# Optimization experiments

Measured on AMD Instinct MI355X. Metric: run time of the kernel, lower is better.

## Reference

```python
import jax, jax.numpy as jnp
import numpy as np

B, T, TA = 16, 512, 1024
D_REG, D_AUD, HID, HEADS = 512, 512, 256, 4
NREG = 4  # mouth, left_eye, right_eye, nose (dict order)
N = NREG * B * T + B * TA  # total graph nodes


def _build_edges():
    # Faithful, vectorized version of build_graph's edge construction (phoneme_times=None).
    bs = np.arange(B)[:, None]
    ts = np.arange(T)[None, :]
    src, dst = [], []
    # cross-region same-timestep edges, all ordered pairs i != j (edge_attr 0)
    for i in range(NREG):
        for j in range(NREG):
            if i != j:
                n1 = i * B * T + bs * T + ts
                n2 = j * B * T + bs * T + ts
                src.append(n1.ravel()); dst.append(n2.ravel())
    # temporal edges within each region (edge_attr 1)
    tt = np.arange(T - 1)[None, :]
    for i in range(NREG):
        n1 = i * B * T + bs * T + tt
        src.append(n1.ravel()); dst.append((n1 + 1).ravel())
    # eye (region idx 1,2) -> audio alignment edges (edge_attr 3)
    t_aud = (np.arange(T)[None, :] * TA) // T
    audio_start = NREG * B * T
    for i in (1, 2):
        n_eye = i * B * T + bs * T + ts
        n_aud = audio_start + bs * TA + t_aud
        src.append(n_eye.ravel()); dst.append(np.broadcast_to(n_aud, (B, T)).ravel())
    # self loops (PyG GATConv default add_self_loops=True)
    loops = np.arange(N)
    src.append(loops); dst.append(loops)
    return np.concatenate(src).astype(np.int32), np.concatenate(dst).astype(np.int32)


def setup_inputs() -> dict:
    key = jax.random.key(0)
    ks = iter(jax.random.split(key, 48))
    def rn(shape, scale=1.0):
        return jax.random.normal(next(ks), shape, dtype=jnp.float32) * jnp.float32(scale)
    src_np, dst_np = _build_edges()
    inp = {
        'mouth': rn((B, T, D_REG)), 'left_eye': rn((B, T, D_REG)),
        'right_eye': rn((B, T, D_REG)), 'nose': rn((B, T, D_REG)),
        'audio_embeddings': rn((B, TA, D_AUD)),
    }
    s = 1.0 / np.sqrt(D_REG)
    for name in ['mouth', 'left_eye', 'right_eye', 'nose']:
        inp['w_' + name] = rn((D_REG, HID), s)
        inp['b_' + name] = jnp.zeros((HID,), jnp.float32)
    inp['w_audio'] = rn((D_AUD, HID), 1.0 / np.sqrt(D_AUD))
    inp['b_audio'] = jnp.zeros((HID,), jnp.float32)
    # GAT layers: layer 0 in=HID, layers 1,2 in=HID*HEADS; layers 0,1 concat, layer 2 averages heads
    dims_in = [HID, HID * HEADS, HID * HEADS]
    for l, din in enumerate(dims_in):
        concat = l < 2
        inp[f'W{l}'] = rn((din, HEADS * HID), 1.0 / np.sqrt(din))
        inp[f'as{l}'] = rn((HEADS, HID), 0.1)
        inp[f'ad{l}'] = rn((HEADS, HID), 0.1)
        inp[f'bias{l}'] = jnp.zeros((HEADS * HID,) if concat else (HID,), jnp.float32)
    inp['ln_g'] = jnp.ones((HID,), jnp.float32)
    inp['ln_b'] = jnp.zeros((HID,), jnp.float32)
    inp['src'] = jnp.asarray(src_np)
    inp['dst'] = jnp.asarray(dst_np)
    return inp


def _gat(x, W, a_s, a_d, bias, src, dst, concat):
    # PyG GATConv (eval mode): gather -> per-head attention softmax over dst -> scatter-add
    H, C = a_s.shape
    h = (x @ W).reshape(-1, H, C)                      # [N,H,C]
    alpha_s = jnp.sum(h * a_s, -1)                     # [N,H]
    alpha_d = jnp.sum(h * a_d, -1)                     # [N,H]
    e = jax.nn.leaky_relu(alpha_s[src] + alpha_d[dst], 0.2)  # [E,H]
    m = jax.ops.segment_max(e, dst, num_segments=N)
    ex = jnp.exp(e - m[dst])
    denom = jax.ops.segment_sum(ex, dst, num_segments=N)
    alpha = ex / (denom[dst] + jnp.float32(1e-16))
    out = jax.ops.segment_sum(h[src] * alpha[:, :, None], dst, num_segments=N)  # [N,H,C]
    out = out.reshape(-1, H * C) if concat else out.mean(1)
    return out + bias


def _forward(mouth, left_eye, right_eye, nose, audio_embeddings,
             w_mouth, b_mouth, w_left_eye, b_left_eye, w_right_eye, b_right_eye,
             w_nose, b_nose, w_audio, b_audio,
             W0, as0, ad0, bias0, W1, as1, ad1, bias1, W2, as2, ad2, bias2,
             ln_g, ln_b, src, dst):
    x = jnp.concatenate([
        (mouth @ w_mouth + b_mouth).reshape(B * T, HID),
        (left_eye @ w_left_eye + b_left_eye).reshape(B * T, HID),
        (right_eye @ w_right_eye + b_right_eye).reshape(B * T, HID),
        (nose @ w_nose + b_nose).reshape(B * T, HID),
        (audio_embeddings @ w_audio + b_audio).reshape(B * TA, HID),
    ], axis=0)                                          # [N,HID]
    x = _gat(x, W0, as0, ad0, bias0, src, dst, True)    # [N,HID*HEADS]
    x = _gat(x, W1, as1, ad1, bias1, src, dst, True)    # [N,HID*HEADS]
    x = _gat(x, W2, as2, ad2, bias2, src, dst, False)   # [N,HID]
    mu = x.mean(-1, keepdims=True)
    var = jnp.mean(jnp.square(x - mu), -1, keepdims=True)
    x = (x - mu) / jnp.sqrt(var + jnp.float32(1e-5)) * ln_g + ln_b
    nodes_pb = NREG * T + TA
    return x.reshape(B, nodes_pb, HID).mean(1)          # [B,HID]


def reference(mouth, left_eye, right_eye, nose, audio_embeddings,
              w_mouth, b_mouth, w_left_eye, b_left_eye, w_right_eye, b_right_eye,
              w_nose, b_nose, w_audio, b_audio,
              W0, as0, ad0, bias0, W1, as1, ad1, bias1, W2, as2, ad2, bias2,
              ln_g, ln_b, src, dst):
    return _forward(mouth, left_eye, right_eye, nose, audio_embeddings,
                    w_mouth, b_mouth, w_left_eye, b_left_eye, w_right_eye, b_right_eye,
                    w_nose, b_nose, w_audio, b_audio,
                    W0, as0, ad0, bias0, W1, as1, ad1, bias1, W2, as2, ad2, bias2,
                    ln_g, ln_b, src, dst)
```

## Files before the change

kernel.cpp:

```cpp
#include <hip/hip_runtime.h>


typedef unsigned short u16;
typedef unsigned int u32;
typedef __bf16 bf16x8 __attribute__((ext_vector_type(8)));
typedef float f32x4 __attribute__((ext_vector_type(4)));

#define ASYNC16(gp, lp)                                                        \
  __builtin_amdgcn_global_load_lds(                                            \
      (const __attribute__((address_space(1))) void*)(gp),                     \
      (__attribute__((address_space(3))) void*)(lp), 16, 0, 0)

__device__ __forceinline__ u16 f2bf(float f) {
  union { float f; u32 u; } v; v.f = f;
  u32 u = v.u + 0x7FFFu + ((v.u >> 16) & 1u);
  return (u16)(u >> 16);
}
__device__ __forceinline__ float bf2f(u16 x) {
  union { u32 u; float f; } v; v.u = ((u32)x) << 16;
  return v.f;
}
__device__ __forceinline__ float4 load_bf4(const u16* p) {
  ushort4 s = *(const ushort4*)p;
  float4 r; r.x = bf2f(s.x); r.y = bf2f(s.y); r.z = bf2f(s.z); r.w = bf2f(s.w);
  return r;
}
__device__ __forceinline__ float lrelu(float v) { return v > 0.f ? v : 0.2f * v; }
__device__ __forceinline__ float dot4(float4 a, float4 b) {
  return a.x * b.x + a.y * b.y + a.z * b.z + a.w * b.w;
}
__device__ __forceinline__ float wred(float v) {
#pragma unroll
  for (int off = 32; off; off >>= 1) v += __shfl_down(v, off);
  return v;
}
__device__ __forceinline__ float wredx(float v) {
#pragma unroll
  for (int off = 32; off; off >>= 1) v += __shfl_xor(v, off);
  return v;
}

struct PK { const float* W[8]; u16* P[8]; int KB[8]; int NN[8]; int st[9]; };
__global__ __launch_bounds__(256) void pack_kernel(PK p) {
  const int f = blockIdx.x * 4 + (threadIdx.x >> 6);
  const int lane = threadIdx.x & 63;
  int e = 0;
  while (f >= p.st[e + 1]) ++e;
  const int local = f - p.st[e];
  const int KB = p.KB[e], N = p.NN[e];
  const int nt = local / KB, kb = local % KB;
  const float* W = p.W[e] + (size_t)(kb * 32 + (lane >> 4) * 8) * N + nt * 16 + (lane & 15);
  u16* dst = p.P[e] + ((size_t)local * 64 + lane) * 8;
  u16 o[8];
#pragma unroll
  for (int j = 0; j < 8; ++j) o[j] = f2bf(W[(size_t)j * N]);
  *(uint4*)dst = *(uint4*)o;
}

__global__ __launch_bounds__(256) void gemm_kernel(
    const u16* __restrict__ A, const u16* __restrict__ Bp, u16* __restrict__ C,
    int K, int ldc) {
  __shared__ __align__(16) u16 As[2][2][128 * 32];
  const int KB = K >> 5;
  const int KB2 = K >> 6;
  const int w = blockIdx.y * 8 + blockIdx.x;
  const int xcd = w & 7, m = w >> 3;
  const int blockCol = (m & 7) * 128;
  const int blockRow = ((m >> 3) * 8 + xcd) * 128;
  const int tid = threadIdx.x;
  const int wave = tid >> 6, lane = tid & 63;
  const int wr = (wave >> 1) * 64, wc = (wave & 1) * 64;
  const int lr = lane & 15, lq = lane >> 4;
  const int sRow = wave * 16 + (lane >> 2);
  const int sGc = (lane & 3) ^ ((sRow >> 1) & 3);
  const size_t aOff0 = (size_t)(blockRow + sRow) * K + sGc * 8;
  const size_t aOff1 = aOff0 + (size_t)64 * K;
  const int ldsOff0 = wave * 512;
  const int ldsOff1 = 2048 + wave * 512;

  const u16* Bn[4];
#pragma unroll
  for (int ni = 0; ni < 4; ++ni)
    Bn[ni] = Bp + ((size_t)(((blockCol + wc) >> 4) + ni) * KB) * 512 + lane * 8;

  f32x4 acc[4][4] = {};

#pragma unroll
  for (int h = 0; h < 2; ++h) {
    ASYNC16(A + aOff0 + h * 32, As[0][h] + ldsOff0);
    ASYNC16(A + aOff1 + h * 32, As[0][h] + ldsOff1);
  }
  __syncthreads();

  for (int kb2 = 0; kb2 < KB2; ++kb2) {
    const int cb = kb2 & 1;
    if (kb2 + 1 < KB2) {
      const size_t k1 = (size_t)(kb2 + 1) * 64;
#pragma unroll
      for (int h = 0; h < 2; ++h) {
        ASYNC16(A + aOff0 + k1 + h * 32, As[cb ^ 1][h] + ldsOff0);
        ASYNC16(A + aOff1 + k1 + h * 32, As[cb ^ 1][h] + ldsOff1);
      }
    }
#pragma unroll
    for (int h = 0; h < 2; ++h) {
      const int kb = kb2 * 2 + h;
      const u16* cur = As[cb][h];
      bf16x8 bfr[4];
#pragma unroll
      for (int ni = 0; ni < 4; ++ni)
        bfr[ni] = *(const bf16x8*)(Bn[ni] + (size_t)kb * 512);
      bf16x8 af[4];
#pragma unroll
      for (int mi = 0; mi < 4; ++mi) {
        const int R = wr + mi * 16 + lr;
        const int cp = lq ^ ((R >> 1) & 3);
        af[mi] = *(const bf16x8*)(cur + R * 32 + cp * 8);
      }
#pragma unroll
      for (int mi = 0; mi < 4; ++mi)
#pragma unroll
        for (int ni = 0; ni < 4; ++ni)
          acc[mi][ni] = __builtin_amdgcn_mfma_f32_16x16x32_bf16(af[mi], bfr[ni],
                                                                acc[mi][ni], 0, 0, 0);
    }
    __syncthreads();
  }
#pragma unroll
  for (int mi = 0; mi < 4; ++mi)
#pragma unroll
    for (int ni = 0; ni < 4; ++ni) {
      const int col = blockCol + wc + ni * 16 + lr;
#pragma unroll
      for (int r = 0; r < 4; ++r) {
        const int row = blockRow + wr + mi * 16 + lq * 4 + r;
        C[(size_t)row * ldc + col] = f2bf(acc[mi][ni][r]);
      }
    }
}

struct ProjArgs { const float* x[5]; const u16* w[5]; const float* b[5]; };
__global__ __launch_bounds__(256) void proj_kernel(ProjArgs pa,
                                                   u16* __restrict__ C) {
  __shared__ __align__(16) u16 As[128 * 32];
  const int blockRow = blockIdx.y * 128, blockCol = blockIdx.x * 128;
  const int reg = blockRow >= 32768 ? 4 : (blockRow >> 13);
  const int regBase = reg == 4 ? 32768 : reg * 8192;
  const float* Af = pa.x[reg] + (size_t)(blockRow - regBase) * 512;
  const u16* Bp = pa.w[reg];
  const int tid = threadIdx.x;
  const int wave = tid >> 6, lane = tid & 63;
  const int wr = (wave >> 1) * 64, wc = (wave & 1) * 64;
  const int lr = lane & 15, lq = lane >> 4;
  const int rr = tid >> 2;
  const int cphys = tid & 3;
  const int sGc = cphys ^ ((tid >> 3) & 3);

  const u16* Bn[4];
#pragma unroll
  for (int ni = 0; ni < 4; ++ni)
    Bn[ni] = Bp + ((size_t)(((blockCol + wc) >> 4) + ni) * 16) * 512 + lane * 8;

  f32x4 acc[4][4] = {};

  for (int k0 = 0; k0 < 512; k0 += 32) {
    __syncthreads();
    bf16x8 bfr[4];
#pragma unroll
    for (int ni = 0; ni < 4; ++ni)
      bfr[ni] = *(const bf16x8*)(Bn[ni] + (size_t)k0 * 16);
#pragma unroll
    for (int i = 0; i < 2; ++i) {
      const int row = i * 64 + rr;
      const float* ap = Af + (size_t)row * 512 + k0 + sGc * 8;
      float4 f0 = *(const float4*)(ap);
      float4 f1 = *(const float4*)(ap + 4);
      uint4 pk;
      pk.x = (u32)f2bf(f0.x) | ((u32)f2bf(f0.y) << 16);
      pk.y = (u32)f2bf(f0.z) | ((u32)f2bf(f0.w) << 16);
      pk.z = (u32)f2bf(f1.x) | ((u32)f2bf(f1.y) << 16);
      pk.w = (u32)f2bf(f1.z) | ((u32)f2bf(f1.w) << 16);
      *(uint4*)(&As[row * 32 + cphys * 8]) = pk;
    }
    __syncthreads();
    bf16x8 af[4];
#pragma unroll
    for (int mi = 0; mi < 4; ++mi) {
      const int R = wr + mi * 16 + lr;
      const int cp = lq ^ ((R >> 1) & 3);
      af[mi] = *(const bf16x8*)(&As[R * 32 + cp * 8]);
    }
#pragma unroll
    for (int mi = 0; mi < 4; ++mi)
#pragma unroll
      for (int ni = 0; ni < 4; ++ni)
        acc[mi][ni] = __builtin_amdgcn_mfma_f32_16x16x32_bf16(af[mi], bfr[ni],
                                                              acc[mi][ni], 0, 0, 0);
  }
  const float* bias = pa.b[reg];
#pragma unroll
  for (int mi = 0; mi < 4; ++mi)
#pragma unroll
    for (int ni = 0; ni < 4; ++ni) {
      const int col = blockCol + wc + ni * 16 + lr;
      const float bv = bias[col];
#pragma unroll
      for (int r = 0; r < 4; ++r) {
        const int row = blockRow + wr + mi * 16 + lq * 4 + r;
        C[(size_t)row * 256 + col] = f2bf(acc[mi][ni][r] + bv);
      }
    }
}

template <bool MEAN>
__global__ __launch_bounds__(256) void agg_kernel(
    const u16* __restrict__ h, const float* __restrict__ a_s,
    const float* __restrict__ a_d, const float* __restrict__ bias,
    const float* __restrict__ lng, const float* __restrict__ lnb,
    void* __restrict__ out) {
  const int tid = threadIdx.x;
  const int head = tid >> 6, lane = tid & 63;
  const int c4 = tid * 4;
  const float4 sa = *(const float4*)(a_s + c4);
  const float4 da = *(const float4*)(a_d + c4);
  __shared__ float asB[2][4][4], adL[4][4], alpha[4][4][5];
  __shared__ float red[MEAN ? 4096 : 1];
  __shared__ float ls[MEAN ? 32 : 1];

  if (blockIdx.x < 1024) {
    const int b = blockIdx.x >> 6;
    const int t0 = (blockIdx.x & 63) * 8;
    float4 hprev[4] = {};
    if (t0 > 0) {
      const int btp = b * 512 + t0 - 1;
#pragma unroll
      for (int r = 0; r < 4; ++r) {
        hprev[r] = load_bf4(h + (size_t)(r * 8192 + btp) * 1024 + c4);
        float sp = wred(dot4(hprev[r], sa));
        if (lane == 0) asB[1][r][head] = sp;
      }
    }
    __syncthreads();
    float pacc[4] = {};
    int pch[4] = {-1, -1, -1, -1};
    for (int tt = 0; tt < 8; ++tt) {
      const int t = t0 + tt, bt = b * 512 + t;
      const bool hasPrev = (t > 0);
      float4 hv[4];
#pragma unroll
      for (int r = 0; r < 4; ++r) {
        hv[r] = load_bf4(h + (size_t)(r * 8192 + bt) * 1024 + c4);
        float ss = wred(dot4(hv[r], sa));
        float dd = wred(dot4(hv[r], da));
        if (lane == 0) { asB[tt & 1][r][head] = ss; adL[r][head] = dd; }
      }
      __syncthreads();
      if (tid < 16) {
        const int j = tid >> 2, hh = tid & 3;
        const float ad = adL[j][hh];
        float e[5];
#pragma unroll
        for (int r = 0; r < 4; ++r) e[r] = lrelu(asB[tt & 1][r][hh] + ad);
        int cnt = 4;
        if (hasPrev) { e[4] = lrelu(asB[(tt & 1) ^ 1][j][hh] + ad); cnt = 5; }
        float mx = e[0];
        for (int k = 1; k < cnt; ++k) mx = fmaxf(mx, e[k]);
        float s = 0.f, ex[5];
        for (int k = 0; k < cnt; ++k) { ex[k] = __expf(e[k] - mx); s += ex[k]; }
        const float inv = 1.f / (s + 1e-16f);
#pragma unroll
        for (int k = 0; k < 5; ++k) alpha[j][hh][k] = (k < cnt) ? ex[k] * inv : 0.f;
      }
      __syncthreads();
#pragma unroll
      for (int j = 0; j < 4; ++j) {
        const float* al = &alpha[j][head][0];
        float4 acc;
        acc.x = al[0] * hv[0].x + al[1] * hv[1].x + al[2] * hv[2].x + al[3] * hv[3].x;
        acc.y = al[0] * hv[0].y + al[1] * hv[1].y + al[2] * hv[2].y + al[3] * hv[3].y;
        acc.z = al[0] * hv[0].z + al[1] * hv[1].z + al[2] * hv[2].z + al[3] * hv[3].z;
        acc.w = al[0] * hv[0].w + al[1] * hv[1].w + al[2] * hv[2].w + al[3] * hv[3].w;
        if (hasPrev) {
          const float a4 = al[4];
          acc.x += a4 * hprev[j].x; acc.y += a4 * hprev[j].y;
          acc.z += a4 * hprev[j].z; acc.w += a4 * hprev[j].w;
        }
        if constexpr (!MEAN) {
          const float4 bv = *(const float4*)(bias + c4);
          ushort4 o;
          o.x = f2bf(acc.x + bv.x); o.y = f2bf(acc.y + bv.y);
          o.z = f2bf(acc.z + bv.z); o.w = f2bf(acc.w + bv.w);
          *(ushort4*)((u16*)out + (size_t)(j * 8192 + bt) * 1024 + c4) = o;
        } else {
          *(float4*)(&red[j * 1024 + c4]) = acc;
        }
      }
      if constexpr (MEAN) {
        __syncthreads();
        const float bb = bias[tid];
        float v[4];
#pragma unroll
        for (int j = 0; j < 4; ++j) {
          v[j] = 0.25f * (red[j * 1024 + tid] + red[j * 1024 + tid + 256] +
                          red[j * 1024 + tid + 512] + red[j * 1024 + tid + 768]) + bb;
          const float sj = wredx(v[j]);
          const float qj = wredx(v[j] * v[j]);
          if (lane == 0) { ls[head * 8 + j * 2] = sj; ls[head * 8 + j * 2 + 1] = qj; }
        }
        __syncthreads();
#pragma unroll
        for (int j = 0; j < 4; ++j) {
          const float S = ls[j * 2] + ls[8 + j * 2] + ls[16 + j * 2] + ls[24 + j * 2];
          const float Q = ls[j * 2 + 1] + ls[8 + j * 2 + 1] + ls[16 + j * 2 + 1] +
                          ls[24 + j * 2 + 1];
          const float mean = S * (1.f / 256.f);
          const float var = Q * (1.f / 256.f) - mean * mean;
          const float n = (v[j] - mean) * rsqrtf(var + 1e-5f) * lng[tid] + lnb[tid];
          const int ch = (j * 8192 + bt) / 3072;
          if (ch != pch[j]) {
            if (pch[j] >= 0) atomicAdd((float*)out + pch[j] * 256 + tid, pacc[j]);
            pacc[j] = 0.f; pch[j] = ch;
          }
          pacc[j] += n;
        }
      }
#pragma unroll
      for (int r = 0; r < 4; ++r) hprev[r] = hv[r];
    }
    if constexpr (MEAN) {
#pragma unroll
      for (int j = 0; j < 4; ++j)
        if (pch[j] >= 0) atomicAdd((float*)out + pch[j] * 256 + tid, pacc[j]);
    }
  } else {
    const int aid = blockIdx.x - 1024;
    const int idx0 = aid * 2;
    const int b = idx0 >> 10;
    const int ta0 = idx0 & 1023;
    const int n0 = 32768 + idx0, n1 = n0 + 1;
    const int tt2 = ta0 >> 1;
    const int le = 8192 + b * 512 + tt2;
    const int re = 16384 + b * 512 + tt2;
    float4 v0 = load_bf4(h + (size_t)n0 * 1024 + c4);
    float4 vo = load_bf4(h + (size_t)n1 * 1024 + c4);
    float4 v1 = load_bf4(h + (size_t)le * 1024 + c4);
    float4 v2 = load_bf4(h + (size_t)re * 1024 + c4);
    {
      float s0 = wred(dot4(v0, sa));
      float s1 = wred(dot4(v1, sa));
      float s2 = wred(dot4(v2, sa));
      float d0 = wred(dot4(v0, da));
      if (lane == 0) {
        asB[0][0][head] = s0; asB[0][1][head] = s1; asB[0][2][head] = s2;
        adL[0][head] = d0;
      }
    }
    __syncthreads();
    if (tid < 4) {
      const float ad = adL[0][tid];
      float e0 = lrelu(asB[0][0][tid] + ad);
      float e1 = lrelu(asB[0][1][tid] + ad);
      float e2 = lrelu(asB[0][2][tid] + ad);
      float mx = fmaxf(e0, fmaxf(e1, e2));
      float x0 = __expf(e0 - mx), x1 = __expf(e1 - mx), x2 = __expf(e2 - mx);
      float inv = 1.f / (x0 + x1 + x2 + 1e-16f);
      alpha[0][tid][0] = x0 * inv; alpha[0][tid][1] = x1 * inv;
      alpha[0][tid][2] = x2 * inv;
    }
    __syncthreads();
    const float a0 = alpha[0][head][0], a1 = alpha[0][head][1], a2 = alpha[0][head][2];
    v0.x = a0 * v0.x + a1 * v1.x + a2 * v2.x;
    v0.y = a0 * v0.y + a1 * v1.y + a2 * v2.y;
    v0.z = a0 * v0.z + a1 * v1.z + a2 * v2.z;
    v0.w = a0 * v0.w + a1 * v1.w + a2 * v2.w;
    if constexpr (!MEAN) {
      const float4 bv = *(const float4*)(bias + c4);
      ushort4 oe, oo;
      oe.x = f2bf(v0.x + bv.x); oe.y = f2bf(v0.y + bv.y);
      oe.z = f2bf(v0.z + bv.z); oe.w = f2bf(v0.w + bv.w);
      oo.x = f2bf(vo.x + bv.x); oo.y = f2bf(vo.y + bv.y);
      oo.z = f2bf(vo.z + bv.z); oo.w = f2bf(vo.w + bv.w);
      *(ushort4*)((u16*)out + (size_t)n0 * 1024 + c4) = oe;
      *(ushort4*)((u16*)out + (size_t)n1 * 1024 + c4) = oo;
    } else {
      *(float4*)(&red[c4]) = v0;
      *(float4*)(&red[1024 + c4]) = vo;
      __syncthreads();
      const float bb = bias[tid];
      float vA = 0.25f * (red[tid] + red[tid + 256] + red[tid + 512] + red[tid + 768]) + bb;
      float vB = 0.25f * (red[1024 + tid] + red[1024 + tid + 256] +
                          red[1024 + tid + 512] + red[1024 + tid + 768]) + bb;
      const float sA = wredx(vA), qA = wredx(vA * vA);
      const float sB = wredx(vB), qB = wredx(vB * vB);
      if (lane == 0) {
        ls[head * 8] = sA; ls[head * 8 + 1] = qA;
        ls[head * 8 + 2] = sB; ls[head * 8 + 3] = qB;
      }
      __syncthreads();
      const float SA = ls[0] + ls[8] + ls[16] + ls[24];
      const float QA = ls[1] + ls[9] + ls[17] + ls[25];
      const float SB = ls[2] + ls[10] + ls[18] + ls[26];
      const float QB = ls[3] + ls[11] + ls[19] + ls[27];
      const float mA = SA * (1.f / 256.f), vrA = QA * (1.f / 256.f) - mA * mA;
      const float mB = SB * (1.f / 256.f), vrB = QB * (1.f / 256.f) - mB * mB;
      const float g = lng[tid], be = lnb[tid];
      const float nA = (vA - mA) * rsqrtf(vrA + 1e-5f) * g + be;
      const float nB = (vB - mB) * rsqrtf(vrB + 1e-5f) * g + be;
      const int ch0 = n0 / 3072, ch1 = n1 / 3072;
      if (ch0 == ch1) {
        atomicAdd((float*)out + ch0 * 256 + tid, nA + nB);
      } else {
        atomicAdd((float*)out + ch0 * 256 + tid, nA);
        atomicAdd((float*)out + ch1 * 256 + tid, nB);
      }
    }
  }
}

__global__ __launch_bounds__(256) void zero_kernel(float* __restrict__ p) {
  p[blockIdx.x * 256 + threadIdx.x] = 0.f;
}
__global__ __launch_bounds__(256) void scale_kernel(float* __restrict__ p) {
  const int i = blockIdx.x * 256 + threadIdx.x;
  p[i] *= (1.f / 3072.f);
}

extern "C" void kernel_launch(void* const* d_in, const int* in_sizes, int n_in,
                              void* d_out, int out_size, void* d_ws, size_t ws_size,
                              hipStream_t stream) {
  const float* x_reg[4] = {(const float*)d_in[0], (const float*)d_in[1],
                           (const float*)d_in[2], (const float*)d_in[3]};
  const float* audio = (const float*)d_in[4];
  const float* w_reg[4] = {(const float*)d_in[5], (const float*)d_in[7],
                           (const float*)d_in[9], (const float*)d_in[11]};
  const float* b_reg[4] = {(const float*)d_in[6], (const float*)d_in[8],
                           (const float*)d_in[10], (const float*)d_in[12]};
  const float* w_aud = (const float*)d_in[13];
  const float* b_aud = (const float*)d_in[14];
  const float* Wl[3] = {(const float*)d_in[15], (const float*)d_in[19],
                        (const float*)d_in[23]};
  const float* as_in[3] = {(const float*)d_in[16], (const float*)d_in[20],
                           (const float*)d_in[24]};
  const float* ad_in[3] = {(const float*)d_in[17], (const float*)d_in[21],
                           (const float*)d_in[25]};
  const float* bias_l[3] = {(const float*)d_in[18], (const float*)d_in[22],
                            (const float*)d_in[26]};
  const float* ln_g = (const float*)d_in[27];
  const float* ln_b = (const float*)d_in[28];

  char* ws = (char*)d_ws;
  u16* h_bf = (u16*)ws;
  u16* xb = (u16*)(ws + 100663296);
  u16* wt = (u16*)(ws + 201326592);

  u16* wtp[5];
  for (int r = 0; r < 5; ++r) wtp[r] = wt + (size_t)r * 131072;
  u16* wt0 = wt + 655360;
  u16* wt1 = wt + 917504;
  u16* wt2 = wt + 1966080;

  PK pk;
  for (int r = 0; r < 4; ++r) { pk.W[r] = w_reg[r]; pk.P[r] = wtp[r]; pk.KB[r] = 16; pk.NN[r] = 256; }
  pk.W[4] = w_aud; pk.P[4] = wtp[4]; pk.KB[4] = 16; pk.NN[4] = 256;
  pk.W[5] = Wl[0]; pk.P[5] = wt0; pk.KB[5] = 8;  pk.NN[5] = 1024;
  pk.W[6] = Wl[1]; pk.P[6] = wt1; pk.KB[6] = 32; pk.NN[6] = 1024;
  pk.W[7] = Wl[2]; pk.P[7] = wt2; pk.KB[7] = 32; pk.NN[7] = 1024;
  pk.st[0] = 0;
  {
    const int nfr[8] = {256, 256, 256, 256, 256, 512, 2048, 2048};
    int acc = 0;
    for (int e = 0; e < 8; ++e) { acc += nfr[e]; pk.st[e + 1] = acc; }
  }
  pack_kernel<<<pk.st[8] / 4, 256, 0, stream>>>(pk);
  zero_kernel<<<16, 256, 0, stream>>>((float*)d_out);

  ProjArgs pa;
  for (int r = 0; r < 4; ++r) { pa.x[r] = x_reg[r]; pa.w[r] = wtp[r]; pa.b[r] = b_reg[r]; }
  pa.x[4] = audio; pa.w[4] = wtp[4]; pa.b[4] = b_aud;
  proj_kernel<<<dim3(2, 384), 256, 0, stream>>>(pa, xb);

  const u16* wl[3] = {wt0, wt1, wt2};
  const int Kl[3] = {256, 1024, 1024};
  for (int l = 0; l < 3; ++l) {
    gemm_kernel<<<dim3(8, 384), 256, 0, stream>>>(xb, wl[l], h_bf, Kl[l], 1024);
    if (l < 2)
      agg_kernel<false><<<9216, 256, 0, stream>>>(h_bf, as_in[l], ad_in[l],
                                                  bias_l[l], nullptr, nullptr, xb);
    else
      agg_kernel<true><<<9216, 256, 0, stream>>>(h_bf, as_in[l], ad_in[l],
                                                 bias_l[l], ln_g, ln_b, d_out);
  }

  scale_kernel<<<16, 256, 0, stream>>>((float*)d_out);
}
```

Before: 687.8 us.

## Compute GAT attention softmax redundantly per wave, drop barriers, prefetch next timestep

The aggregation kernel now has every wave compute its head's attention scores with xor-shuffle reductions and evaluate the softmax in registers. This removes the shared-memory staging and the two block barriers per timestep. It also software-prefetches the next timestep's bf16 rows and halves the timesteps per block (4 instead of 8), doubling the region blocks to raise parallelism. The trade-off is redundant exp and softmax math in every lane, more registers, and one extra halo row load per block.

```diff
diff --git a/kernel.cpp b/kernel.cpp
--- a/kernel.cpp
+++ b/kernel.cpp
@@ -20,19 +20,16 @@
   union { u32 u; float f; } v; v.u = ((u32)x) << 16;
   return v.f;
 }
-__device__ __forceinline__ float4 load_bf4(const u16* p) {
-  ushort4 s = *(const ushort4*)p;
+__device__ __forceinline__ float4 cvt4(ushort4 s) {
   float4 r; r.x = bf2f(s.x); r.y = bf2f(s.y); r.z = bf2f(s.z); r.w = bf2f(s.w);
   return r;
+}
+__device__ __forceinline__ float4 load_bf4(const u16* p) {
+  return cvt4(*(const ushort4*)p);
 }
 __device__ __forceinline__ float lrelu(float v) { return v > 0.f ? v : 0.2f * v; }
 __device__ __forceinline__ float dot4(float4 a, float4 b) {
   return a.x * b.x + a.y * b.y + a.z * b.z + a.w * b.w;
-}
-__device__ __forceinline__ float wred(float v) {
-#pragma unroll
-  for (int off = 32; off; off >>= 1) v += __shfl_down(v, off);
-  return v;
 }
 __device__ __forceinline__ float wredx(float v) {
 #pragma unroll
@@ -219,83 +216,91 @@
     const float* __restrict__ lng, const float* __restrict__ lnb,
     void* __restrict__ out) {
   const int tid = threadIdx.x;
-  const int head = tid >> 6, lane = tid & 63;
+  const int head = tid >> 6;
   const int c4 = tid * 4;
   const float4 sa = *(const float4*)(a_s + c4);
   const float4 da = *(const float4*)(a_d + c4);
-  __shared__ float asB[2][4][4], adL[4][4], alpha[4][4][5];
-  __shared__ float red[MEAN ? 4096 : 1];
-  __shared__ float ls[MEAN ? 32 : 1];
-
-  if (blockIdx.x < 1024) {
-    const int b = blockIdx.x >> 6;
-    const int t0 = (blockIdx.x & 63) * 8;
-    float4 hprev[4] = {};
+
+  if (blockIdx.x < 2048) {
+    const int b = blockIdx.x >> 7;
+    const int t0 = (blockIdx.x & 127) * 4;
+    const int btBase = b * 512 + t0;
+    float4 hprev[4];
+    float ssPrev[4] = {};
     if (t0 > 0) {
-      const int btp = b * 512 + t0 - 1;
-#pragma unroll
-      for (int r = 0; r < 4; ++r) {
-        hprev[r] = load_bf4(h + (size_t)(r * 8192 + btp) * 1024 + c4);
-        float sp = wred(dot4(hprev[r], sa));
-        if (lane == 0) asB[1][r][head] = sp;
-      }
-    }
-    __syncthreads();
+#pragma unroll
+      for (int r = 0; r < 4; ++r)
+        hprev[r] = load_bf4(h + (size_t)(r * 8192 + btBase - 1) * 1024 + c4);
+#pragma unroll
+      for (int r = 0; r < 4; ++r) ssPrev[r] = wredx(dot4(hprev[r], sa));
+    }
+    ushort4 rcur[4];
+#pragma unroll
+    for (int r = 0; r < 4; ++r)
+      rcur[r] = *(const ushort4*)(h + (size_t)(r * 8192 + btBase) * 1024 + c4);
+
     float pacc[4] = {};
     int pch[4] = {-1, -1, -1, -1};
-    for (int tt = 0; tt < 8; ++tt) {
-      const int t = t0 + tt, bt = b * 512 + t;
-      const bool hasPrev = (t > 0);
+
+    for (int tt = 0; tt < 4; ++tt) {
+      const int bt = btBase + tt;
+      const bool hasPrev = (t0 + tt) > 0;
+      ushort4 rnxt[4];
+      if (tt < 3) {
+#pragma unroll
+        for (int r = 0; r < 4; ++r)
+          rnxt[r] = *(const ushort4*)(h + (size_t)(r * 8192 + bt + 1) * 1024 + c4);
+      }
       float4 hv[4];
 #pragma unroll
+      for (int r = 0; r < 4; ++r) hv[r] = cvt4(rcur[r]);
+      float ss[4], dd[4];
+#pragma unroll
       for (int r = 0; r < 4; ++r) {
-        hv[r] = load_bf4(h + (size_t)(r * 8192 + bt) * 1024 + c4);
-        float ss = wred(dot4(hv[r], sa));
-        float dd = wred(dot4(hv[r], da));
-        if (lane == 0) { asB[tt & 1][r][head] = ss; adL[r][head] = dd; }
-      }
-      __syncthreads();
-      if (tid < 16) {
-        const int j = tid >> 2, hh = tid & 3;
-        const float ad = adL[j][hh];
-        float e[5];
-#pragma unroll
-        for (int r = 0; r < 4; ++r) e[r] = lrelu(asB[tt & 1][r][hh] + ad);
-        int cnt = 4;
-        if (hasPrev) { e[4] = lrelu(asB[(tt & 1) ^ 1][j][hh] + ad); cnt = 5; }
-        float mx = e[0];
-        for (int k = 1; k < cnt; ++k) mx = fmaxf(mx, e[k]);
-        float s = 0.f, ex[5];
-        for (int k = 0; k < cnt; ++k) { ex[k] = __expf(e[k] - mx); s += ex[k]; }
-        const float inv = 1.f / (s + 1e-16f);
-#pragma unroll
-        for (int k = 0; k < 5; ++k) alpha[j][hh][k] = (k < cnt) ? ex[k] * inv : 0.f;
-      }
-      __syncthreads();
+        ss[r] = wredx(dot4(hv[r], sa));
+        dd[r] = wredx(dot4(hv[r], da));
+      }
+      float4 av[4];
 #pragma unroll
       for (int j = 0; j < 4; ++j) {
-        const float* al = &alpha[j][head][0];
+        const float ad = dd[j];
+        float e0 = lrelu(ss[0] + ad), e1 = lrelu(ss[1] + ad);
+        float e2 = lrelu(ss[2] + ad), e3 = lrelu(ss[3] + ad);
+        float mx = fmaxf(fmaxf(e0, e1), fmaxf(e2, e3));
+        float e4 = 0.f;
+        if (hasPrev) { e4 = lrelu(ssPrev[j] + ad); mx = fmaxf(mx, e4); }
+        const float x0 = __expf(e0 - mx), x1 = __expf(e1 - mx);
+        const float x2 = __expf(e2 - mx), x3 = __expf(e3 - mx);
+        const float x4 = hasPrev ? __expf(e4 - mx) : 0.f;
+        const float inv = 1.f / (x0 + x1 + x2 + x3 + x4 + 1e-16f);
+        const float a0 = x0 * inv, a1 = x1 * inv, a2 = x2 * inv, a3 = x3 * inv;
+        const float a4 = x4 * inv;
         float4 acc;
-        acc.x = al[0] * hv[0].x + al[1] * hv[1].x + al[2] * hv[2].x + al[3] * hv[3].x;
-        acc.y = al[0] * hv[0].y + al[1] * hv[1].y + al[2] * hv[2].y + al[3] * hv[3].y;
-        acc.z = al[0] * hv[0].z + al[1] * hv[1].z + al[2] * hv[2].z + al[3] * hv[3].z;
-        acc.w = al[0] * hv[0].w + al[1] * hv[1].w + al[2] * hv[2].w + al[3] * hv[3].w;
+        acc.x = a0 * hv[0].x + a1 * hv[1].x + a2 * hv[2].x + a3 * hv[3].x;
+        acc.y = a0 * hv[0].y + a1 * hv[1].y + a2 * hv[2].y + a3 * hv[3].y;
+        acc.z = a0 * hv[0].z + a1 * hv[1].z + a2 * hv[2].z + a3 * hv[3].z;
+        acc.w = a0 * hv[0].w + a1 * hv[1].w + a2 * hv[2].w + a3 * hv[3].w;
         if (hasPrev) {
-          const float a4 = al[4];
           acc.x += a4 * hprev[j].x; acc.y += a4 * hprev[j].y;
           acc.z += a4 * hprev[j].z; acc.w += a4 * hprev[j].w;
         }
-        if constexpr (!MEAN) {
-          const float4 bv = *(const float4*)(bias + c4);
+        av[j] = acc;
+      }
+      if constexpr (!MEAN) {
+        const float4 bv = *(const float4*)(bias + c4);
+        u16* ob = (u16*)out;
+#pragma unroll
+        for (int j = 0; j < 4; ++j) {
           ushort4 o;
-          o.x = f2bf(acc.x + bv.x); o.y = f2bf(acc.y + bv.y);
-          o.z = f2bf(acc.z + bv.z); o.w = f2bf(acc.w + bv.w);
-          *(ushort4*)((u16*)out + (size_t)(j * 8192 + bt) * 1024 + c4) = o;
-        } else {
-          *(float4*)(&red[j * 1024 + c4]) = acc;
+          o.x = f2bf(av[j].x + bv.x); o.y = f2bf(av[j].y + bv.y);
+          o.z = f2bf(av[j].z + bv.z); o.w = f2bf(av[j].w + bv.w);
+          *(ushort4*)(ob + (size_t)(j * 8192 + bt) * 1024 + c4) = o;
         }
-      }
-      if constexpr (MEAN) {
+      } else {
+        __shared__ float red[4096];
+        __shared__ float ls[32];
+#pragma unroll
+        for (int j = 0; j < 4; ++j) *(float4*)(&red[j * 1024 + c4]) = av[j];
         __syncthreads();
         const float bb = bias[tid];
         float v[4];
@@ -305,7 +310,7 @@
                           red[j * 1024 + tid + 512] + red[j * 1024 + tid + 768]) + bb;
           const float sj = wredx(v[j]);
           const float qj = wredx(v[j] * v[j]);
-          if (lane == 0) { ls[head * 8 + j * 2] = sj; ls[head * 8 + j * 2 + 1] = qj; }
+          if ((tid & 63) == 0) { ls[head * 8 + j * 2] = sj; ls[head * 8 + j * 2 + 1] = qj; }
         }
         __syncthreads();
 #pragma unroll
@@ -325,7 +330,11 @@
         }
       }
 #pragma unroll
-      for (int r = 0; r < 4; ++r) hprev[r] = hv[r];
+      for (int r = 0; r < 4; ++r) {
+        hprev[r] = hv[r];
+        ssPrev[r] = ss[r];
+        rcur[r] = rnxt[r];
+      }
     }
     if constexpr (MEAN) {
 #pragma unroll
@@ -333,7 +342,7 @@
         if (pch[j] >= 0) atomicAdd((float*)out + pch[j] * 256 + tid, pacc[j]);
     }
   } else {
-    const int aid = blockIdx.x - 1024;
+    const int aid = blockIdx.x - 2048;
     const int idx0 = aid * 2;
     const int b = idx0 >> 10;
     const int ta0 = idx0 & 1023;
@@ -345,34 +354,21 @@
     float4 vo = load_bf4(h + (size_t)n1 * 1024 + c4);
     float4 v1 = load_bf4(h + (size_t)le * 1024 + c4);
     float4 v2 = load_bf4(h + (size_t)re * 1024 + c4);
+    const float s0 = wredx(dot4(v0, sa));
+    const float s1 = wredx(dot4(v1, sa));
+    const float s2 = wredx(dot4(v2, sa));
+    const float d0 = wredx(dot4(v0, da));
     {
-      float s0 = wred(dot4(v0, sa));
-      float s1 = wred(dot4(v1, sa));
-      float s2 = wred(dot4(v2, sa));
-      float d0 = wred(dot4(v0, da));
-      if (lane == 0) {
-        asB[0][0][head] = s0; asB[0][1][head] = s1; asB[0][2][head] = s2;
-        adL[0][head] = d0;
-      }
-    }
-    __syncthreads();
-    if (tid < 4) {
-      const float ad = adL[0][tid];
-      float e0 = lrelu(asB[0][0][tid] + ad);
-      float e1 = lrelu(asB[0][1][tid] + ad);
-      float e2 = lrelu(asB[0][2][tid] + ad);
-      float mx = fmaxf(e0, fmaxf(e1, e2));
-      float x0 = __expf(e0 - mx), x1 = __expf(e1 - mx), x2 = __expf(e2 - mx);
-      float inv = 1.f / (x0 + x1 + x2 + 1e-16f);
-      alpha[0][tid][0] = x0 * inv; alpha[0][tid][1] = x1 * inv;
-      alpha[0][tid][2] = x2 * inv;
-    }
-    __syncthreads();
-    const float a0 = alpha[0][head][0], a1 = alpha[0][head][1], a2 = alpha[0][head][2];
-    v0.x = a0 * v0.x + a1 * v1.x + a2 * v2.x;
-    v0.y = a0 * v0.y + a1 * v1.y + a2 * v2.y;
-    v0.z = a0 * v0.z + a1 * v1.z + a2 * v2.z;
-    v0.w = a0 * v0.w + a1 * v1.w + a2 * v2.w;
+      const float e0 = lrelu(s0 + d0), e1 = lrelu(s1 + d0), e2 = lrelu(s2 + d0);
+      const float mx = fmaxf(e0, fmaxf(e1, e2));
+      const float x0 = __expf(e0 - mx), x1 = __expf(e1 - mx), x2 = __expf(e2 - mx);
+      const float inv = 1.f / (x0 + x1 + x2 + 1e-16f);
+      const float a0 = x0 * inv, a1 = x1 * inv, a2 = x2 * inv;
+      v0.x = a0 * v0.x + a1 * v1.x + a2 * v2.x;
+      v0.y = a0 * v0.y + a1 * v1.y + a2 * v2.y;
+      v0.z = a0 * v0.z + a1 * v1.z + a2 * v2.z;
+      v0.w = a0 * v0.w + a1 * v1.w + a2 * v2.w;
+    }
     if constexpr (!MEAN) {
       const float4 bv = *(const float4*)(bias + c4);
       ushort4 oe, oo;
@@ -383,24 +379,27 @@
       *(ushort4*)((u16*)out + (size_t)n0 * 1024 + c4) = oe;
       *(ushort4*)((u16*)out + (size_t)n1 * 1024 + c4) = oo;
     } else {
-      *(float4*)(&red[c4]) = v0;
-      *(float4*)(&red[1024 + c4]) = vo;
+      __shared__ float redA[2048];
+      __shared__ float lsA[32];
+      *(float4*)(&redA[c4]) = v0;
+      *(float4*)(&redA[1024 + c4]) = vo;
       __syncthreads();
       const float bb = bias[tid];
-      float vA = 0.25f * (red[tid] + red[tid + 256] + red[tid + 512] + red[tid + 768]) + bb;
-      float vB = 0.25f * (red[1024 + tid] + red[1024 + tid + 256] +
-                          red[1024 + tid + 512] + red[1024 + tid + 768]) + bb;
+      float vA = 0.25f * (redA[tid] + redA[tid + 256] + redA[tid + 512] +
+                          redA[tid + 768]) + bb;
+      float vB = 0.25f * (redA[1024 + tid] + redA[1024 + tid + 256] +
+                          redA[1024 + tid + 512] + redA[1024 + tid + 768]) + bb;
       const float sA = wredx(vA), qA = wredx(vA * vA);
       const float sB = wredx(vB), qB = wredx(vB * vB);
-      if (lane == 0) {
-        ls[head * 8] = sA; ls[head * 8 + 1] = qA;
-        ls[head * 8 + 2] = sB; ls[head * 8 + 3] = qB;
+      if ((tid & 63) == 0) {
+        lsA[head * 8] = sA; lsA[head * 8 + 1] = qA;
+        lsA[head * 8 + 2] = sB; lsA[head * 8 + 3] = qB;
       }
       __syncthreads();
-      const float SA = ls[0] + ls[8] + ls[16] + ls[24];
-      const float QA = ls[1] + ls[9] + ls[17] + ls[25];
-      const float SB = ls[2] + ls[10] + ls[18] + ls[26];
-      const float QB = ls[3] + ls[11] + ls[19] + ls[27];
+      const float SA = lsA[0] + lsA[8] + lsA[16] + lsA[24];
+      const float QA = lsA[1] + lsA[9] + lsA[17] + lsA[25];
+      const float SB = lsA[2] + lsA[10] + lsA[18] + lsA[26];
+      const float QB = lsA[3] + lsA[11] + lsA[19] + lsA[27];
       const float mA = SA * (1.f / 256.f), vrA = QA * (1.f / 256.f) - mA * mA;
       const float mB = SB * (1.f / 256.f), vrB = QB * (1.f / 256.f) - mB * mB;
       const float g = lng[tid], be = lnb[tid];
@@ -484,11 +483,11 @@
   for (int l = 0; l < 3; ++l) {
     gemm_kernel<<<dim3(8, 384), 256, 0, stream>>>(xb, wl[l], h_bf, Kl[l], 1024);
     if (l < 2)
-      agg_kernel<false><<<9216, 256, 0, stream>>>(h_bf, as_in[l], ad_in[l],
-                                                  bias_l[l], nullptr, nullptr, xb);
+      agg_kernel<false><<<10240, 256, 0, stream>>>(h_bf, as_in[l], ad_in[l],
+                                                   bias_l[l], nullptr, nullptr, xb);
     else
-      agg_kernel<true><<<9216, 256, 0, stream>>>(h_bf, as_in[l], ad_in[l],
-                                                 bias_l[l], ln_g, ln_b, d_out);
+      agg_kernel<true><<<10240, 256, 0, stream>>>(h_bf, as_in[l], ad_in[l],
+                                                  bias_l[l], ln_g, ln_b, d_out);
   }
 
   scale_kernel<<<16, 256, 0, stream>>>((float*)d_out);
```

After: 710.7 us. 1.03x slower.
